# Optimization experiments

Measured on AMD Instinct MI355X. Metric: run time of the kernel, lower is better.

Reference implementation:

```python
import jax, jax.numpy as jnp
import numpy as np

W = 10        # hurst window == signature path window (increments)
DELTA_MAX = 1.5
BN_EPS = 1e-5


def _revcumsum(x, axis):
    return jnp.flip(jnp.cumsum(jnp.flip(x, axis), axis=axis), axis)


def _forward(features, hw1, hb1, hw2, hb2, hw3, hb3, gw1, gb1, gw2, gb2,
             p1, p1b, p2, p2b, p3, p3b, p4, p4b,
             w1, b1, gamma, beta, rmean, rvar, w2, b2, w3, b3):
    B, T, d = features.shape
    f32 = features.dtype
    # log returns, left-padded with 0
    lp = features[:, :, 0]
    ret = jnp.pad(lp[:, 1:] - lp[:, :-1], ((0, 0), (1, 0)))
    # Hurst estimator on sliding windows returns[:, t-W:t] for t in [W, T)
    idxh = jnp.arange(T - W)[:, None] + jnp.arange(W)[None, :]
    rw = ret[:, idxh]                                          # [B, T-W, W]
    hh = jax.nn.relu(rw @ hw1 + hb1)
    hh = jax.nn.relu(hh @ hw2 + hb2)
    H_tail = 0.5 * jax.nn.sigmoid((hh @ hw3 + hb3)[..., 0])    # [B, T-W]
    # first W entries copy the t=W estimate (matches torch slice-broadcast)
    H_local = jnp.concatenate([jnp.repeat(H_tail[:, :1], W, axis=1), H_tail], axis=1)
    vol = jnp.cumsum(jnp.abs(ret), axis=1) / (jnp.arange(1, T + 1, dtype=f32) + 1e-8)
    # depth gate from (H_local, vol_local)
    regime = jnp.stack([H_local, vol], axis=-1)                # [B, T, 2]
    gate = jax.nn.softmax(jax.nn.relu(regime @ gw1 + gb1) @ gw2 + gb2, axis=-1)  # [B,T,4]
    # windowed path increments: window at t covers global increments t-W .. t-1
    Dinc = features[:, 1:] - features[:, :-1]                  # [B, T-1, d]
    Dp = jnp.pad(Dinc, ((0, 0), (W, 0), (0, 0)))
    idx = jnp.arange(T)[:, None] + jnp.arange(W)[None, :]
    Dw = Dp[:, idx]                                            # [B, T, W, d] (zero-padded early)
    S = _revcumsum(Dw, 2)                                      # suffix sums S_r = sum_{m>=r} D_m
    lvl1 = S[:, :, 0]                                          # [B, T, d] = path[-1]-path[0]
    # level2 (torch loop) = sum_{i<=m} D_i (x) D_m  (diagonal included)
    A = Dw[..., :, None] * S[..., None, :]                     # [B, T, W, d, d]
    l2f = jnp.sum(A, axis=2).reshape(B, T, d * d)
    # level3 (torch loop) = sum_{i<j<=n} D_i (x) D_j (x) D_n
    RA = _revcumsum(A, 2) - A                                  # exclusive suffix sum of A
    l3f = jnp.einsum('btrd,btref->btdef', Dw, RA).reshape(B, T, d ** 3)
    # level4 = flatten(level2 (x) level2); (d^2)^2 == d^4 so no pad/trunc
    l4f = (l2f[..., :, None] * l2f[..., None, :]).reshape(B, T, d ** 4)
    proj1 = lvl1 @ p1 + p1b
    proj2 = jnp.concatenate([lvl1, l2f], -1) @ p2 + p2b
    proj3 = jnp.concatenate([lvl1, l2f, l3f], -1) @ p3 + p3b
    proj4 = jnp.concatenate([lvl1, l2f, l3f, l4f], -1) @ p4 + p4b
    # depth k active iff path_len >= k+1 i.e. t >= k (k = depth index)
    tv = jnp.arange(T)
    m2 = (tv >= 1).astype(f32)[None, :, None]
    m3 = (tv >= 2).astype(f32)[None, :, None]
    m4 = (tv >= 3).astype(f32)[None, :, None]
    sig_repr = (gate[..., 0:1] * proj1 + m2 * gate[..., 1:2] * proj2
                + m3 * gate[..., 2:3] * proj3 + m4 * gate[..., 3:4] * proj4)
    combined = jnp.concatenate([sig_repr, features], axis=-1)  # [B, T, h+d]
    h1 = jax.nn.relu(combined @ w1 + b1)
    bn = gamma * (h1 - rmean) * jax.lax.rsqrt(rvar + BN_EPS) + beta  # BatchNorm1d (eval)
    h2 = jax.nn.relu(bn @ w2 + b2)
    return DELTA_MAX * jnp.tanh((h2 @ w3 + b3)[..., 0])        # [B, T]


def setup_inputs() -> dict:
    key = jax.random.key(0)
    ks = jax.random.split(key, 24)
    B, T, d, h = 32, 2048, 5, 64
    def w(k, shape, s=0.1):
        return (jax.random.normal(k, shape) * s).astype(jnp.float32)
    z = lambda n: jnp.zeros((n,), jnp.float32)
    return dict(
        features=0.1 * jax.random.normal(ks[0], (B, T, d), jnp.float32),
        hw1=w(ks[1], (10, 32)), hb1=z(32),
        hw2=w(ks[2], (32, 32)), hb2=z(32),
        hw3=w(ks[3], (32, 1)), hb3=z(1),
        gw1=w(ks[4], (2, 32)), gb1=z(32),
        gw2=w(ks[5], (32, 4)), gb2=z(4),
        p1=w(ks[6], (5, h)), p1b=z(h),
        p2=w(ks[7], (30, h)), p2b=z(h),
        p3=w(ks[8], (155, h)), p3b=z(h),
        p4=w(ks[9], (780, h)), p4b=z(h),
        w1=w(ks[10], (h + d, h)), b1=z(h),
        gamma=jnp.ones((h,), jnp.float32), beta=z(h),
        rmean=0.05 * jax.random.normal(ks[11], (h,), dtype=jnp.float32),
        rvar=jax.random.uniform(ks[12], (h,), jnp.float32, 0.5, 1.5),
        w2=w(ks[13], (h, h // 2)), b2=z(h // 2),
        w3=w(ks[14], (h // 2, 1)), b3=z(1),
    )


def reference(features, hw1, hb1, hw2, hb2, hw3, hb3, gw1, gb1, gw2, gb2,
              p1, p1b, p2, p2b, p3, p3b, p4, p4b,
              w1, b1, gamma, beta, rmean, rvar, w2, b2, w3, b3):
    return _forward(features, hw1, hb1, hw2, hb2, hw3, hb3, gw1, gb1, gw2, gb2,
                    p1, p1b, p2, p2b, p3, p3b, p4, p4b,
                    w1, b1, gamma, beta, rmean, rvar, w2, b2, w3, b3)
```

## Files before the change

### kernel.cpp

```cpp
#include <hip/hip_runtime.h>
#include <math.h>

#define TT 2048
#define W 10

typedef short bf16x8 __attribute__((ext_vector_type(8)));
typedef float f32x4 __attribute__((ext_vector_type(4)));

__device__ __forceinline__ void splitTrunc(float v, unsigned short& hi,
                                           unsigned short& lo) {
  unsigned int u = __float_as_uint(v);
  hi = (unsigned short)(u >> 16);
  float r = v - __uint_as_float(u & 0xffff0000u);
  lo = (unsigned short)(__float_as_uint(r) >> 16);
}

__global__ __launch_bounds__(256) void pre_kernel(
    const float* __restrict__ F,
    const float* __restrict__ hw1, const float* __restrict__ hb1,
    const float* __restrict__ hw2, const float* __restrict__ hb2,
    const float* __restrict__ hw3, const float* __restrict__ hb3,
    const float* __restrict__ gw1, const float* __restrict__ gb1,
    const float* __restrict__ gw2, const float* __restrict__ gb2,
    const float* __restrict__ p1, const float* __restrict__ p2,
    const float* __restrict__ p3, const float* __restrict__ p4,
    unsigned short* __restrict__ WtH, unsigned short* __restrict__ WtL,
    float* __restrict__ gate) {
  const int bid = blockIdx.x;
  const int tid = threadIdx.x;
  if (bid >= 256) {
    int g = (bid - 256) * 256 + tid;
    float v;
    if (g < 2048) {
      int h = g >> 5, k = g & 31;
      v = (k < 5) ? p1[k * 64 + h] : 0.f;
    } else if (g < 4096) {
      int loc = g - 2048, h = loc >> 5, k = loc & 31;
      v = (k < 30) ? p2[k * 64 + h] : 0.f;
    } else if (g < 14336) {
      int loc = g - 4096, h = loc / 160, k = loc - h * 160;
      v = (k < 155) ? p3[k * 64 + h] : 0.f;
    } else {
      int loc = g - 14336, h = loc / 800, k = loc - h * 800;
      if (k < 155) v = p4[k * 64 + h];
      else if (k >= 160 && k < 785) v = p4[(k - 5) * 64 + h];
      else v = 0.f;
    }
    unsigned short hi, lo;
    splitTrunc(v, hi, lo);
    WtH[g] = hi;
    WtL[g] = lo;
    return;
  }
  __shared__ float sRet[TT];
  __shared__ float sCum[TT];
  __shared__ float sPart[256];
  const int b = bid >> 3;
  const int t0 = (bid & 7) << 8;
  const float* fb = F + (size_t)b * TT * 5;
#pragma unroll
  for (int u = 0; u < 8; ++u) {
    int t = u * 256 + tid;
    sRet[t] = (t > 0) ? (fb[t * 5] - fb[(t - 1) * 5]) : 0.f;
  }
  __syncthreads();
  float loc8[8], run = 0.f;
#pragma unroll
  for (int u = 0; u < 8; ++u) {
    run += fabsf(sRet[tid * 8 + u]);
    loc8[u] = run;
  }
  sPart[tid] = run;
  __syncthreads();
  for (int off = 1; off < 256; off <<= 1) {
    float v = (tid >= off) ? sPart[tid - off] : 0.f;
    __syncthreads();
    sPart[tid] += v;
    __syncthreads();
  }
  float excl = sPart[tid] - run;
#pragma unroll
  for (int u = 0; u < 8; ++u) sCum[tid * 8 + u] = excl + loc8[u];
  __syncthreads();
  const int t = t0 + tid;
  const float vv = sCum[t] / ((float)(t + 1) + 1e-8f);
  const int start = (t >= W) ? (t - W) : 0;
  float r[W];
#pragma unroll
  for (int u = 0; u < W; ++u) r[u] = sRet[start + u];
  float h1v[32];
#pragma unroll
  for (int j = 0; j < 32; ++j) {
    float a = hb1[j];
#pragma unroll
    for (int u = 0; u < W; ++u) a = fmaf(r[u], hw1[u * 32 + j], a);
    h1v[j] = fmaxf(a, 0.f);
  }
  float hs = hb3[0];
#pragma unroll
  for (int j = 0; j < 32; ++j) {
    float a = hb2[j];
#pragma unroll
    for (int u = 0; u < 32; ++u) a = fmaf(h1v[u], hw2[u * 32 + j], a);
    hs = fmaf(fmaxf(a, 0.f), hw3[j], hs);
  }
  const float H = 0.5f / (1.f + expf(-hs));
  float l0 = gb2[0], l1 = gb2[1], l2 = gb2[2], l3 = gb2[3];
#pragma unroll
  for (int j = 0; j < 32; ++j) {
    float z = fmaxf(fmaf(H, gw1[j], fmaf(vv, gw1[32 + j], gb1[j])), 0.f);
    l0 = fmaf(z, gw2[j * 4 + 0], l0);
    l1 = fmaf(z, gw2[j * 4 + 1], l1);
    l2 = fmaf(z, gw2[j * 4 + 2], l2);
    l3 = fmaf(z, gw2[j * 4 + 3], l3);
  }
  float m = fmaxf(fmaxf(l0, l1), fmaxf(l2, l3));
  float e0 = expf(l0 - m), e1 = expf(l1 - m), e2 = expf(l2 - m),
        e3 = expf(l3 - m);
  float inv = 1.f / (e0 + e1 + e2 + e3);
  ((float4*)gate)[b * TT + t] = make_float4(e0 * inv, e1 * inv, e2 * inv, e3 * inv);
}

#define MFMA16(a, b, c) __builtin_amdgcn_mfma_f32_16x16x32_bf16((a), (b), (c), 0, 0, 0)

__global__ __launch_bounds__(512, 4) void sig_kernel(
    const float* __restrict__ F, const float* __restrict__ gate,
    const unsigned short* __restrict__ WtH, const unsigned short* __restrict__ WtL,
    const float* __restrict__ p1b, const float* __restrict__ p2b,
    const float* __restrict__ p3b, const float* __restrict__ p4b,
    const float* __restrict__ w1, const float* __restrict__ b1,
    const float* __restrict__ gam, const float* __restrict__ bet,
    const float* __restrict__ rmean, const float* __restrict__ rvar,
    const float* __restrict__ w2, const float* __restrict__ b2,
    const float* __restrict__ w3, const float* __restrict__ b3,
    float* __restrict__ out) {
  __shared__ unsigned short phiH[16][808];
  __shared__ unsigned short phiL[16][808];
  __shared__ __align__(16) float sX[3152];
  __shared__ float sFeat[80];

  float* sDw = sX;
  float* sS = sX + 800;
  float* sL2 = sX + 1600;

  const int tid = threadIdx.x;
  const int posBase = blockIdx.x * 16;

  for (int u = tid; u < 800; u += 512) {
    int p = u / 50, rr = u - p * 50;
    int r = rr / 5, i = rr - r * 5;
    int pos = posBase + p;
    int t = pos & (TT - 1);
    int q = t + r - W;
    float dv = 0.f;
    if (q >= 0) {
      const float* fb = F + (size_t)(pos - t) * 5;
      dv = fb[(q + 1) * 5 + i] - fb[q * 5 + i];
    }
    sDw[u] = dv;
  }
  if (tid < 80) sFeat[tid] = F[(size_t)posBase * 5 + tid];
  __syncthreads();

  if (tid < 80) {
    int p = tid / 5, i = tid - (tid / 5) * 5;
    float s = 0.f;
#pragma unroll
    for (int r = W - 1; r >= 0; --r) {
      s += sDw[p * 50 + r * 5 + i];
      sS[p * 50 + r * 5 + i] = s;
    }
    unsigned short hi, lo;
    splitTrunc(s, hi, lo);
    phiH[p][i] = hi;
    phiL[p][i] = lo;
  }
  __syncthreads();

  if (tid < 400) {
    int p = tid / 25, ef = tid - (tid / 25) * 25;
    int e = ef / 5, fi = ef - e * 5;
    const float* dwp = sDw + p * 50;
    const float* sp = sS + p * 50;
    float a = 0.f;
    float l3a[5] = {0.f, 0.f, 0.f, 0.f, 0.f};
#pragma unroll
    for (int r = W - 1; r >= 0; --r) {
      float aa = a;
#pragma unroll
      for (int i = 0; i < 5; ++i) l3a[i] = fmaf(dwp[r * 5 + i], aa, l3a[i]);
      a = fmaf(dwp[r * 5 + e], sp[r * 5 + fi], a);
    }
    sL2[p * 25 + ef] = a;
    unsigned short hi, lo;
    splitTrunc(a, hi, lo);
    phiH[p][5 + ef] = hi;
    phiL[p][5 + ef] = lo;
#pragma unroll
    for (int i = 0; i < 5; ++i) {
      splitTrunc(l3a[i], hi, lo);
      phiH[p][30 + i * 25 + ef] = hi;
      phiL[p][30 + i * 25 + ef] = lo;
    }
  }
  if (tid < 320) {
    int p = tid / 20, mm = tid - (tid / 20) * 20;
    int kk = (mm < 5) ? (155 + mm) : (780 + mm);
    phiH[p][kk] = 0;
    phiL[p][kk] = 0;
  }
  __syncthreads();

  {
    int p = tid >> 5, t32 = tid & 31;
    int base = t32 * 20;
    int count = (t32 == 31) ? 5 : 20;
    const float* l2p = sL2 + p * 25;
    int i = base / 25, j = base - i * 25;
    unsigned short* rowH = &phiH[p][160 + base];
    unsigned short* rowL = &phiL[p][160 + base];
    int mEnd = count & ~1;
    for (int m = 0; m < mEnd; m += 2) {
      float v0 = l2p[i] * l2p[j];
      j++; if (j == 25) { j = 0; i++; }
      float v1 = l2p[i] * l2p[j];
      j++; if (j == 25) { j = 0; i++; }
      unsigned short h0, lo0, h1, lo1;
      splitTrunc(v0, h0, lo0);
      splitTrunc(v1, h1, lo1);
      *(unsigned int*)(rowH + m) = (unsigned int)h0 | ((unsigned int)h1 << 16);
      *(unsigned int*)(rowL + m) = (unsigned int)lo0 | ((unsigned int)lo1 << 16);
    }
    if (count & 1) {
      float v0 = l2p[i] * l2p[j];
      unsigned short h0, lo0;
      splitTrunc(v0, h0, lo0);
      rowH[mEnd] = h0;
      rowL[mEnd] = lo0;
    }
  }
  __syncthreads();

  const int lane = tid & 63;
  const int wvAll = tid >> 6;
  const int ht = wvAll & 3, kg = wvAll >> 2;
  const int col = lane & 15, quad = lane >> 4;
  const int hw = ht * 16;
  const int arow = hw + col;

  const unsigned short* bHp = &phiH[col][quad * 8];
  const unsigned short* bLp = &phiL[col][quad * 8];
  const unsigned short* a4H = WtH + 14336 + arow * 800 + quad * 8;
  const unsigned short* a4L = WtL + 14336 + arow * 800 + quad * 8;

  f32x4 acc4a = {0.f, 0.f, 0.f, 0.f}, acc4b = {0.f, 0.f, 0.f, 0.f};
  f32x4 acc3a = {0.f, 0.f, 0.f, 0.f}, acc3b = {0.f, 0.f, 0.f, 0.f};
  f32x4 acc2 = {0.f, 0.f, 0.f, 0.f}, acc1 = {0.f, 0.f, 0.f, 0.f};

  if (kg == 0) {
    for (int s = 0; s < 16; ++s) {
      bf16x8 bh = *(const bf16x8*)(bHp + s * 32);
      bf16x8 bl = *(const bf16x8*)(bLp + s * 32);
      bf16x8 ah = *(const bf16x8*)(a4H + s * 32);
      bf16x8 al = *(const bf16x8*)(a4L + s * 32);
      acc4a = MFMA16(ah, bh, acc4a);
      acc4b = MFMA16(ah, bl, acc4b);
      acc4b = MFMA16(al, bh, acc4b);
    }
  } else {
    for (int s = 16; s < 25; ++s) {
      bf16x8 bh = *(const bf16x8*)(bHp + s * 32);
      bf16x8 bl = *(const bf16x8*)(bLp + s * 32);
      bf16x8 ah = *(const bf16x8*)(a4H + s * 32);
      bf16x8 al = *(const bf16x8*)(a4L + s * 32);
      acc4a = MFMA16(ah, bh, acc4a);
      acc4b = MFMA16(ah, bl, acc4b);
      acc4b = MFMA16(al, bh, acc4b);
    }
    const unsigned short* a3H = WtH + 4096 + arow * 160 + quad * 8;
    const unsigned short* a3L = WtL + 4096 + arow * 160 + quad * 8;
    for (int s = 0; s < 5; ++s) {
      bf16x8 bh = *(const bf16x8*)(bHp + s * 32);
      bf16x8 bl = *(const bf16x8*)(bLp + s * 32);
      bf16x8 ch = *(const bf16x8*)(a3H + s * 32);
      bf16x8 cl = *(const bf16x8*)(a3L + s * 32);
      acc3a = MFMA16(ch, bh, acc3a);
      acc3b = MFMA16(ch, bl, acc3b);
      acc3b = MFMA16(cl, bh, acc3b);
    }
    bf16x8 bh0 = *(const bf16x8*)(bHp);
    bf16x8 bl0 = *(const bf16x8*)(bLp);
    const unsigned short* a2H = WtH + 2048 + arow * 32 + quad * 8;
    const unsigned short* a2L = WtL + 2048 + arow * 32 + quad * 8;
    bf16x8 dh = *(const bf16x8*)a2H;
    bf16x8 dl = *(const bf16x8*)a2L;
    acc2 = MFMA16(dh, bh0, acc2);
    acc2 = MFMA16(dh, bl0, acc2);
    acc2 = MFMA16(dl, bh0, acc2);
    const unsigned short* a1H = WtH + arow * 32 + quad * 8;
    const unsigned short* a1L = WtL + arow * 32 + quad * 8;
    bf16x8 eh = *(const bf16x8*)a1H;
    bf16x8 el = *(const bf16x8*)a1L;
    acc1 = MFMA16(eh, bh0, acc1);
    acc1 = MFMA16(eh, bl0, acc1);
    acc1 = MFMA16(el, bh0, acc1);
  }

  const int pos = posBase + col;
  const int t = pos & (TT - 1);
  float4 g = ((const float4*)gate)[pos];
  const float g0 = g.x;
  const float g1 = (t >= 1) ? g.y : 0.f;
  const float g2 = (t >= 2) ? g.z : 0.f;
  const float g3 = (t >= 3) ? g.w : 0.f;

  if (kg == 1) {
    f32x4 a4 = acc4a + acc4b;
    f32x4 a3 = acc3a + acc3b;
    f32x4 v;
#pragma unroll
    for (int r = 0; r < 4; ++r)
      v[r] = g0 * acc1[r] + g1 * acc2[r] + g2 * a3[r] + g3 * a4[r];
    *(f32x4*)&sX[(ht * 64 + lane) * 4] = v;
  }
  __syncthreads();
  if (kg == 0) {
    f32x4 a4 = acc4a + acc4b;
    f32x4 vo = *(const f32x4*)&sX[(ht * 64 + lane) * 4];
    float* sSig = sX + 1024;
#pragma unroll
    for (int r = 0; r < 4; ++r) {
      int h = hw + quad * 4 + r;
      float bias = g0 * p1b[h] + g1 * p2b[h] + g2 * p3b[h] + g3 * p4b[h];
      sSig[col * 68 + h] = vo[r] + g3 * a4[r] + bias;
    }
  }
  __syncthreads();

  {
    const float* sSig = sX + 1024;
    float* sBn = sX + 2112;
    const int j = lane;
    const int pA = wvAll * 2, pB = pA + 1;
    float a0 = b1[j], a1 = a0;
    const float* sg0 = sSig + pA * 68;
    const float* sg1 = sSig + pB * 68;
    for (int i = 0; i < 64; ++i) {
      float wt = w1[i * 64 + j];
      a0 = fmaf(sg0[i], wt, a0);
      a1 = fmaf(sg1[i], wt, a1);
    }
#pragma unroll
    for (int i = 0; i < 5; ++i) {
      float wt = w1[(64 + i) * 64 + j];
      a0 = fmaf(sFeat[pA * 5 + i], wt, a0);
      a1 = fmaf(sFeat[pB * 5 + i], wt, a1);
    }
    float sc = gam[j] * rsqrtf(rvar[j] + 1e-5f);
    float rm = rmean[j], be = bet[j];
    sBn[pA * 65 + j] = fmaf(fmaxf(a0, 0.f) - rm, sc, be);
    sBn[pB * 65 + j] = fmaf(fmaxf(a1, 0.f) - rm, sc, be);
  }
  __syncthreads();

  {
    const float* sBn = sX + 2112;
    const float b3s = b3[0];
    int p = tid >> 5, k = tid & 31;
    const float* bnp = sBn + p * 65;
    float a = b2[k];
    for (int jj = 0; jj < 64; ++jj) a = fmaf(bnp[jj], w2[jj * 32 + k], a);
    float partial = fmaxf(a, 0.f) * w3[k];
#pragma unroll
    for (int off = 16; off >= 1; off >>= 1) partial += __shfl_xor(partial, off, 32);
    if (k == 0) out[posBase + p] = 1.5f * tanhf(partial + b3s);
  }
}

extern "C" void kernel_launch(void* const* d_in, const int* in_sizes, int n_in,
                              void* d_out, int out_size, void* d_ws, size_t ws_size,
                              hipStream_t stream) {
  const float* F = (const float*)d_in[0];
  const float* hw1 = (const float*)d_in[1];
  const float* hb1 = (const float*)d_in[2];
  const float* hw2 = (const float*)d_in[3];
  const float* hb2 = (const float*)d_in[4];
  const float* hw3 = (const float*)d_in[5];
  const float* hb3 = (const float*)d_in[6];
  const float* gw1 = (const float*)d_in[7];
  const float* gb1 = (const float*)d_in[8];
  const float* gw2 = (const float*)d_in[9];
  const float* gb2 = (const float*)d_in[10];
  const float* p1 = (const float*)d_in[11];
  const float* p1b = (const float*)d_in[12];
  const float* p2 = (const float*)d_in[13];
  const float* p2b = (const float*)d_in[14];
  const float* p3 = (const float*)d_in[15];
  const float* p3b = (const float*)d_in[16];
  const float* p4 = (const float*)d_in[17];
  const float* p4b = (const float*)d_in[18];
  const float* w1 = (const float*)d_in[19];
  const float* b1 = (const float*)d_in[20];
  const float* gam = (const float*)d_in[21];
  const float* bet = (const float*)d_in[22];
  const float* rmean = (const float*)d_in[23];
  const float* rvar = (const float*)d_in[24];
  const float* w2 = (const float*)d_in[25];
  const float* b2 = (const float*)d_in[26];
  const float* w3 = (const float*)d_in[27];
  const float* b3 = (const float*)d_in[28];

  float* ws = (float*)d_ws;
  float* gate = ws;
  unsigned short* WtH = (unsigned short*)(ws + 262144);
  unsigned short* WtL = WtH + 65536;
  float* out = (float*)d_out;

  pre_kernel<<<512, 256, 0, stream>>>(F, hw1, hb1, hw2, hb2, hw3, hb3, gw1,
                                      gb1, gw2, gb2, p1, p2, p3, p4, WtH, WtL,
                                      gate);
  sig_kernel<<<4096, 512, 0, stream>>>(F, gate, WtH, WtL, p1b, p2b, p3b, p4b,
                                       w1, b1, gam, bet, rmean, rvar, w2, b2,
                                       w3, b3, out);
}
```

Measured before the change: 241.7 us.

## Exploit symmetry of level-2 outer product to halve level-4 GEMM K dimension

The level-4 signature features are the outer product of the level-2 vector with itself, which is symmetric. The p4 weights are therefore folded so only 13 of the 25 cyclic diagonals are used, shrinking the K dimension from 800 to 512 and cutting LDS and MFMA work. Signature levels are now computed from raw features in registers with one wave per position, and the l2xl2 products are built with cross-lane shuffles. The change also removes a sync stage, shrinks LDS to allow 6 blocks per CU, and switches the bf16 hi/lo split from truncation to round-to-nearest.

Result: slower. 253.3 us (+4.8%).

```diff
diff --git a/kernel.cpp b/kernel.cpp
--- a/kernel.cpp
+++ b/kernel.cpp
@@ -7,13 +7,24 @@
 typedef short bf16x8 __attribute__((ext_vector_type(8)));
 typedef float f32x4 __attribute__((ext_vector_type(4)));
 
-__device__ __forceinline__ void splitTrunc(float v, unsigned short& hi,
-                                           unsigned short& lo) {
+#define MFMA16(a, b, c) __builtin_amdgcn_mfma_f32_16x16x32_bf16((a), (b), (c), 0, 0, 0)
+
+__device__ __forceinline__ unsigned short rneBf16(float v) {
   unsigned int u = __float_as_uint(v);
-  hi = (unsigned short)(u >> 16);
-  float r = v - __uint_as_float(u & 0xffff0000u);
-  lo = (unsigned short)(__float_as_uint(r) >> 16);
-}
+  u += 0x7FFFu + ((u >> 16) & 1u);
+  return (unsigned short)(u >> 16);
+}
+__device__ __forceinline__ void splitRne(float v, unsigned short& hi,
+                                         unsigned short& lo) {
+  hi = rneBf16(v);
+  float r = v - __uint_as_float((unsigned int)hi << 16);
+  lo = rneBf16(r);
+}
+
+#define OFF_W2 2048
+#define OFF_W3 4096
+#define OFF_W4 14336
+#define WT_TOTAL 47104
 
 __global__ __launch_bounds__(256) void pre_kernel(
     const float* __restrict__ F,
@@ -41,13 +52,22 @@
       int loc = g - 4096, h = loc / 160, k = loc - h * 160;
       v = (k < 155) ? p3[k * 64 + h] : 0.f;
     } else {
-      int loc = g - 14336, h = loc / 800, k = loc - h * 800;
-      if (k < 155) v = p4[k * 64 + h];
-      else if (k >= 160 && k < 785) v = p4[(k - 5) * 64 + h];
-      else v = 0.f;
+      int loc = g - 14336, h = loc >> 9, k = loc & 511;
+      if (k < 155) {
+        v = p4[k * 64 + h];
+      } else if (k >= 160 && k < 485) {
+        int kap = k - 160;
+        int c = kap / 25, mm = kap - c * 25;
+        int jj = mm + c;
+        if (jj >= 25) jj -= 25;
+        v = p4[(155 + mm * 25 + jj) * 64 + h];
+        if (c > 0) v += p4[(155 + jj * 25 + mm) * 64 + h];
+      } else {
+        v = 0.f;
+      }
     }
     unsigned short hi, lo;
-    splitTrunc(v, hi, lo);
+    splitRne(v, hi, lo);
     WtH[g] = hi;
     WtL[g] = lo;
     return;
@@ -121,9 +141,44 @@
   ((float4*)gate)[b * TT + t] = make_float4(e0 * inv, e1 * inv, e2 * inv, e3 * inv);
 }
 
-#define MFMA16(a, b, c) __builtin_amdgcn_mfma_f32_16x16x32_bf16((a), (b), (c), 0, 0, 0)
-
-__global__ __launch_bounds__(512, 4) void sig_kernel(
+template <bool GUARD>
+static __device__ __forceinline__ void sigCore(const float* sR, int p, int e,
+                                               int fi, float* l3a, float& aout,
+                                               float& sout) {
+  int b10 = (p + 10) * 5;
+  float h0 = sR[b10 + 0], h1 = sR[b10 + 1], h2 = sR[b10 + 2], h3 = sR[b10 + 3],
+        h4 = sR[b10 + 4];
+  float hiE = sR[b10 + e], hiF = sR[b10 + fi];
+  float a = 0.f, sfi = 0.f;
+  float l0 = 0.f, l1 = 0.f, l2 = 0.f, l3 = 0.f, l4 = 0.f;
+#pragma unroll
+  for (int r = 9; r >= 0; --r) {
+    const int base = (p + r) * 5;
+    float n0 = sR[base + 0], n1 = sR[base + 1], n2 = sR[base + 2],
+          n3 = sR[base + 3], n4 = sR[base + 4];
+    float nE = sR[base + e], nF = sR[base + fi];
+    float d0 = h0 - n0, d1 = h1 - n1, d2 = h2 - n2, d3 = h3 - n3, d4 = h4 - n4;
+    float dE = hiE - nE, dF = hiF - nF;
+    if (GUARD) {
+      float vm = ((p + r) >= 10) ? 1.f : 0.f;
+      d0 *= vm; d1 *= vm; d2 *= vm; d3 *= vm; d4 *= vm; dE *= vm; dF *= vm;
+    }
+    sfi += dF;
+    float aa = a;
+    l0 = fmaf(d0, aa, l0);
+    l1 = fmaf(d1, aa, l1);
+    l2 = fmaf(d2, aa, l2);
+    l3 = fmaf(d3, aa, l3);
+    l4 = fmaf(d4, aa, l4);
+    a = fmaf(dE, sfi, a);
+    h0 = n0; h1 = n1; h2 = n2; h3 = n3; h4 = n4; hiE = nE; hiF = nF;
+  }
+  l3a[0] = l0; l3a[1] = l1; l3a[2] = l2; l3a[3] = l3; l3a[4] = l4;
+  aout = a;
+  sout = sfi;
+}
+
+__global__ __launch_bounds__(512, 6) void sig_kernel(
     const float* __restrict__ F, const float* __restrict__ gate,
     const unsigned short* __restrict__ WtH, const unsigned short* __restrict__ WtL,
     const float* __restrict__ p1b, const float* __restrict__ p2b,
@@ -134,164 +189,141 @@
     const float* __restrict__ w2, const float* __restrict__ b2,
     const float* __restrict__ w3, const float* __restrict__ b3,
     float* __restrict__ out) {
-  __shared__ unsigned short phiH[16][808];
-  __shared__ unsigned short phiL[16][808];
-  __shared__ __align__(16) float sX[3152];
-  __shared__ float sFeat[80];
-
-  float* sDw = sX;
-  float* sS = sX + 800;
-  float* sL2 = sX + 1600;
+  __shared__ __align__(16) unsigned short phiH[16][520];
+  __shared__ __align__(16) unsigned short phiL[16][520];
+  __shared__ float sRaw[132];
 
   const int tid = threadIdx.x;
   const int posBase = blockIdx.x * 16;
-
-  for (int u = tid; u < 800; u += 512) {
-    int p = u / 50, rr = u - p * 50;
-    int r = rr / 5, i = rr - r * 5;
-    int pos = posBase + p;
-    int t = pos & (TT - 1);
-    int q = t + r - W;
-    float dv = 0.f;
-    if (q >= 0) {
-      const float* fb = F + (size_t)(pos - t) * 5;
-      dv = fb[(q + 1) * 5 + i] - fb[q * 5 + i];
-    }
-    sDw[u] = dv;
-  }
-  if (tid < 80) sFeat[tid] = F[(size_t)posBase * 5 + tid];
-  __syncthreads();
-
-  if (tid < 80) {
-    int p = tid / 5, i = tid - (tid / 5) * 5;
-    float s = 0.f;
-#pragma unroll
-    for (int r = W - 1; r >= 0; --r) {
-      s += sDw[p * 50 + r * 5 + i];
-      sS[p * 50 + r * 5 + i] = s;
-    }
-    unsigned short hi, lo;
-    splitTrunc(s, hi, lo);
-    phiH[p][i] = hi;
-    phiL[p][i] = lo;
-  }
-  __syncthreads();
-
-  if (tid < 400) {
-    int p = tid / 25, ef = tid - (tid / 25) * 25;
-    int e = ef / 5, fi = ef - e * 5;
-    const float* dwp = sDw + p * 50;
-    const float* sp = sS + p * 50;
-    float a = 0.f;
-    float l3a[5] = {0.f, 0.f, 0.f, 0.f, 0.f};
-#pragma unroll
-    for (int r = W - 1; r >= 0; --r) {
-      float aa = a;
-#pragma unroll
-      for (int i = 0; i < 5; ++i) l3a[i] = fmaf(dwp[r * 5 + i], aa, l3a[i]);
-      a = fmaf(dwp[r * 5 + e], sp[r * 5 + fi], a);
-    }
-    sL2[p * 25 + ef] = a;
-    unsigned short hi, lo;
-    splitTrunc(a, hi, lo);
-    phiH[p][5 + ef] = hi;
-    phiL[p][5 + ef] = lo;
-#pragma unroll
-    for (int i = 0; i < 5; ++i) {
-      splitTrunc(l3a[i], hi, lo);
-      phiH[p][30 + i * 25 + ef] = hi;
-      phiL[p][30 + i * 25 + ef] = lo;
-    }
-  }
-  if (tid < 320) {
-    int p = tid / 20, mm = tid - (tid / 20) * 20;
-    int kk = (mm < 5) ? (155 + mm) : (780 + mm);
+  const int t0 = posBase & (TT - 1);
+
+  {
+    int p = tid >> 5, mm = tid & 31;
+    int kk = (mm < 5) ? (155 + mm) : (480 + mm);
     phiH[p][kk] = 0;
     phiL[p][kk] = 0;
   }
-  __syncthreads();
-
-  {
-    int p = tid >> 5, t32 = tid & 31;
-    int base = t32 * 20;
-    int count = (t32 == 31) ? 5 : 20;
-    const float* l2p = sL2 + p * 25;
-    int i = base / 25, j = base - i * 25;
-    unsigned short* rowH = &phiH[p][160 + base];
-    unsigned short* rowL = &phiL[p][160 + base];
-    int mEnd = count & ~1;
-    for (int m = 0; m < mEnd; m += 2) {
-      float v0 = l2p[i] * l2p[j];
-      j++; if (j == 25) { j = 0; i++; }
-      float v1 = l2p[i] * l2p[j];
-      j++; if (j == 25) { j = 0; i++; }
-      unsigned short h0, lo0, h1, lo1;
-      splitTrunc(v0, h0, lo0);
-      splitTrunc(v1, h1, lo1);
-      *(unsigned int*)(rowH + m) = (unsigned int)h0 | ((unsigned int)h1 << 16);
-      *(unsigned int*)(rowL + m) = (unsigned int)lo0 | ((unsigned int)lo1 << 16);
-    }
-    if (count & 1) {
-      float v0 = l2p[i] * l2p[j];
-      unsigned short h0, lo0;
-      splitTrunc(v0, h0, lo0);
-      rowH[mEnd] = h0;
-      rowL[mEnd] = lo0;
+  if (tid < 130) {
+    const float* fb = F + (size_t)(posBase - t0) * 5;
+    int idx = (t0 - W) * 5 + tid;
+    sRaw[tid] = (idx >= 0) ? fb[idx] : 0.f;
+  }
+  __syncthreads();
+
+  const int pgrp = tid >> 5;
+  const int m = tid & 31;
+  float l2v = 0.f;
+  if (m < 25) {
+    const int e = m / 5;
+    const int fi = m - e * 5;
+    float l3a[5], a, sfi;
+    if (t0 != 0)
+      sigCore<false>(sRaw, pgrp, e, fi, l3a, a, sfi);
+    else
+      sigCore<true>(sRaw, pgrp, e, fi, l3a, a, sfi);
+    l2v = a;
+    unsigned short hi, lo;
+    if (m < 5) {
+      splitRne(sfi, hi, lo);
+      phiH[pgrp][m] = hi;
+      phiL[pgrp][m] = lo;
+    }
+    splitRne(a, hi, lo);
+    phiH[pgrp][5 + m] = hi;
+    phiL[pgrp][5 + m] = lo;
+#pragma unroll
+    for (int i = 0; i < 5; ++i) {
+      splitRne(l3a[i], hi, lo);
+      phiH[pgrp][30 + i * 25 + m] = hi;
+      phiL[pgrp][30 + i * 25 + m] = lo;
+    }
+  }
+  const int laneBase = tid & 32;
+#pragma unroll
+  for (int c = 0; c < 13; ++c) {
+    int j = m + c;
+    if (j >= 25) j -= 25;
+    float other = __shfl(l2v, laneBase + j, 64);
+    if (m < 25) {
+      unsigned short hi, lo;
+      splitRne(l2v * other, hi, lo);
+      phiH[pgrp][160 + c * 25 + m] = hi;
+      phiL[pgrp][160 + c * 25 + m] = lo;
     }
   }
   __syncthreads();
 
   const int lane = tid & 63;
-  const int wvAll = tid >> 6;
-  const int ht = wvAll & 3, kg = wvAll >> 2;
+  const int wv = tid >> 6;
+  const int ht = wv & 3, kg = wv >> 2;
   const int col = lane & 15, quad = lane >> 4;
   const int hw = ht * 16;
   const int arow = hw + col;
 
   const unsigned short* bHp = &phiH[col][quad * 8];
   const unsigned short* bLp = &phiL[col][quad * 8];
-  const unsigned short* a4H = WtH + 14336 + arow * 800 + quad * 8;
-  const unsigned short* a4L = WtL + 14336 + arow * 800 + quad * 8;
-
-  f32x4 acc4a = {0.f, 0.f, 0.f, 0.f}, acc4b = {0.f, 0.f, 0.f, 0.f};
-  f32x4 acc3a = {0.f, 0.f, 0.f, 0.f}, acc3b = {0.f, 0.f, 0.f, 0.f};
-  f32x4 acc2 = {0.f, 0.f, 0.f, 0.f}, acc1 = {0.f, 0.f, 0.f, 0.f};
-
+  const unsigned short* a4H = WtH + OFF_W4 + arow * 512 + quad * 8;
+  const unsigned short* a4L = WtL + OFF_W4 + arow * 512 + quad * 8;
+
+  const int pos = posBase + col;
+  const int t = pos & (TT - 1);
+  float4 g = ((const float4*)gate)[pos];
+  const float g0 = g.x;
+  const float g1 = (t >= 1) ? g.y : 0.f;
+  const float g2 = (t >= 2) ? g.z : 0.f;
+  const float g3 = (t >= 3) ? g.w : 0.f;
+
+  f32x4 res;
   if (kg == 0) {
-    for (int s = 0; s < 16; ++s) {
+    f32x4 t4a = {0.f, 0.f, 0.f, 0.f}, t4b = {0.f, 0.f, 0.f, 0.f};
+    for (int s = 0; s < 12; ++s) {
       bf16x8 bh = *(const bf16x8*)(bHp + s * 32);
       bf16x8 bl = *(const bf16x8*)(bLp + s * 32);
       bf16x8 ah = *(const bf16x8*)(a4H + s * 32);
       bf16x8 al = *(const bf16x8*)(a4L + s * 32);
-      acc4a = MFMA16(ah, bh, acc4a);
-      acc4b = MFMA16(ah, bl, acc4b);
-      acc4b = MFMA16(al, bh, acc4b);
-    }
+      t4a = MFMA16(ah, bh, t4a);
+      t4b = MFMA16(ah, bl, t4b);
+      t4b = MFMA16(al, bh, t4b);
+    }
+    f32x4 a4 = t4a + t4b;
+    const int hq = hw + quad * 4;
+    f32x4 b1v = *(const f32x4*)(p1b + hq);
+    f32x4 b2v = *(const f32x4*)(p2b + hq);
+    f32x4 b3v = *(const f32x4*)(p3b + hq);
+    f32x4 b4v = *(const f32x4*)(p4b + hq);
+#pragma unroll
+    for (int r = 0; r < 4; ++r)
+      res[r] = g3 * a4[r] + g0 * b1v[r] + g1 * b2v[r] + g2 * b3v[r] + g3 * b4v[r];
   } else {
-    for (int s = 16; s < 25; ++s) {
+    f32x4 t4a = {0.f, 0.f, 0.f, 0.f}, t4b = {0.f, 0.f, 0.f, 0.f};
+    for (int s = 12; s < 16; ++s) {
       bf16x8 bh = *(const bf16x8*)(bHp + s * 32);
       bf16x8 bl = *(const bf16x8*)(bLp + s * 32);
       bf16x8 ah = *(const bf16x8*)(a4H + s * 32);
       bf16x8 al = *(const bf16x8*)(a4L + s * 32);
-      acc4a = MFMA16(ah, bh, acc4a);
-      acc4b = MFMA16(ah, bl, acc4b);
-      acc4b = MFMA16(al, bh, acc4b);
-    }
-    const unsigned short* a3H = WtH + 4096 + arow * 160 + quad * 8;
-    const unsigned short* a3L = WtL + 4096 + arow * 160 + quad * 8;
+      t4a = MFMA16(ah, bh, t4a);
+      t4b = MFMA16(ah, bl, t4b);
+      t4b = MFMA16(al, bh, t4b);
+    }
+    f32x4 a4 = t4a + t4b;
+    const unsigned short* a3H = WtH + OFF_W3 + arow * 160 + quad * 8;
+    const unsigned short* a3L = WtL + OFF_W3 + arow * 160 + quad * 8;
+    f32x4 t3a = {0.f, 0.f, 0.f, 0.f}, t3b = {0.f, 0.f, 0.f, 0.f};
     for (int s = 0; s < 5; ++s) {
       bf16x8 bh = *(const bf16x8*)(bHp + s * 32);
       bf16x8 bl = *(const bf16x8*)(bLp + s * 32);
       bf16x8 ch = *(const bf16x8*)(a3H + s * 32);
       bf16x8 cl = *(const bf16x8*)(a3L + s * 32);
-      acc3a = MFMA16(ch, bh, acc3a);
-      acc3b = MFMA16(ch, bl, acc3b);
-      acc3b = MFMA16(cl, bh, acc3b);
-    }
+      t3a = MFMA16(ch, bh, t3a);
+      t3b = MFMA16(ch, bl, t3b);
+      t3b = MFMA16(cl, bh, t3b);
+    }
+    f32x4 a3 = t3a + t3b;
     bf16x8 bh0 = *(const bf16x8*)(bHp);
     bf16x8 bl0 = *(const bf16x8*)(bLp);
-    const unsigned short* a2H = WtH + 2048 + arow * 32 + quad * 8;
-    const unsigned short* a2L = WtL + 2048 + arow * 32 + quad * 8;
+    f32x4 acc2 = {0.f, 0.f, 0.f, 0.f}, acc1 = {0.f, 0.f, 0.f, 0.f};
+    const unsigned short* a2H = WtH + OFF_W2 + arow * 32 + quad * 8;
+    const unsigned short* a2L = WtL + OFF_W2 + arow * 32 + quad * 8;
     bf16x8 dh = *(const bf16x8*)a2H;
     bf16x8 dl = *(const bf16x8*)a2L;
     acc2 = MFMA16(dh, bh0, acc2);
@@ -304,70 +336,55 @@
     acc1 = MFMA16(eh, bh0, acc1);
     acc1 = MFMA16(eh, bl0, acc1);
     acc1 = MFMA16(el, bh0, acc1);
-  }
-
-  const int pos = posBase + col;
-  const int t = pos & (TT - 1);
-  float4 g = ((const float4*)gate)[pos];
-  const float g0 = g.x;
-  const float g1 = (t >= 1) ? g.y : 0.f;
-  const float g2 = (t >= 2) ? g.z : 0.f;
-  const float g3 = (t >= 3) ? g.w : 0.f;
-
-  if (kg == 1) {
-    f32x4 a4 = acc4a + acc4b;
-    f32x4 a3 = acc3a + acc3b;
-    f32x4 v;
 #pragma unroll
     for (int r = 0; r < 4; ++r)
-      v[r] = g0 * acc1[r] + g1 * acc2[r] + g2 * a3[r] + g3 * a4[r];
-    *(f32x4*)&sX[(ht * 64 + lane) * 4] = v;
-  }
-  __syncthreads();
-  if (kg == 0) {
-    f32x4 a4 = acc4a + acc4b;
-    f32x4 vo = *(const f32x4*)&sX[(ht * 64 + lane) * 4];
-    float* sSig = sX + 1024;
-#pragma unroll
-    for (int r = 0; r < 4; ++r) {
-      int h = hw + quad * 4 + r;
-      float bias = g0 * p1b[h] + g1 * p2b[h] + g2 * p3b[h] + g3 * p4b[h];
-      sSig[col * 68 + h] = vo[r] + g3 * a4[r] + bias;
-    }
-  }
-  __syncthreads();
-
+      res[r] = g0 * acc1[r] + g1 * acc2[r] + g2 * a3[r] + g3 * a4[r];
+  }
+
+  __syncthreads();
+
+  float* sSigA = (float*)&phiH[0][0];
+  float* sSigB = sSigA + 16 * 66;
   {
-    const float* sSig = sX + 1024;
-    float* sBn = sX + 2112;
+    float* dst = (kg == 0) ? sSigA : sSigB;
+    const int hq = hw + quad * 4;
+#pragma unroll
+    for (int r = 0; r < 4; ++r) dst[col * 66 + hq + r] = res[r];
+  }
+  __syncthreads();
+
+  {
     const int j = lane;
-    const int pA = wvAll * 2, pB = pA + 1;
+    const int pA = wv * 2, pB = pA + 1;
     float a0 = b1[j], a1 = a0;
-    const float* sg0 = sSig + pA * 68;
-    const float* sg1 = sSig + pB * 68;
+    const float* sA0 = sSigA + pA * 66;
+    const float* sB0 = sSigB + pA * 66;
+    const float* sA1 = sSigA + pB * 66;
+    const float* sB1 = sSigB + pB * 66;
     for (int i = 0; i < 64; ++i) {
       float wt = w1[i * 64 + j];
-      a0 = fmaf(sg0[i], wt, a0);
-      a1 = fmaf(sg1[i], wt, a1);
+      a0 = fmaf(sA0[i] + sB0[i], wt, a0);
+      a1 = fmaf(sA1[i] + sB1[i], wt, a1);
     }
 #pragma unroll
     for (int i = 0; i < 5; ++i) {
       float wt = w1[(64 + i) * 64 + j];
-      a0 = fmaf(sFeat[pA * 5 + i], wt, a0);
-      a1 = fmaf(sFeat[pB * 5 + i], wt, a1);
+      a0 = fmaf(sRaw[(10 + pA) * 5 + i], wt, a0);
+      a1 = fmaf(sRaw[(10 + pB) * 5 + i], wt, a1);
     }
     float sc = gam[j] * rsqrtf(rvar[j] + 1e-5f);
     float rm = rmean[j], be = bet[j];
-    sBn[pA * 65 + j] = fmaf(fmaxf(a0, 0.f) - rm, sc, be);
-    sBn[pB * 65 + j] = fmaf(fmaxf(a1, 0.f) - rm, sc, be);
+    float* sBn = (float*)&phiL[0][0];
+    sBn[pA * 64 + j] = fmaf(fmaxf(a0, 0.f) - rm, sc, be);
+    sBn[pB * 64 + j] = fmaf(fmaxf(a1, 0.f) - rm, sc, be);
   }
   __syncthreads();
 
   {
-    const float* sBn = sX + 2112;
+    const float* sBn = (const float*)&phiL[0][0];
     const float b3s = b3[0];
     int p = tid >> 5, k = tid & 31;
-    const float* bnp = sBn + p * 65;
+    const float* bnp = sBn + p * 64;
     float a = b2[k];
     for (int jj = 0; jj < 64; ++jj) a = fmaf(bnp[jj], w2[jj * 32 + k], a);
     float partial = fmaxf(a, 0.f) * w3[k];
@@ -413,10 +430,10 @@
   float* ws = (float*)d_ws;
   float* gate = ws;
   unsigned short* WtH = (unsigned short*)(ws + 262144);
-  unsigned short* WtL = WtH + 65536;
+  unsigned short* WtL = WtH + WT_TOTAL;
   float* out = (float*)d_out;
 
-  pre_kernel<<<512, 256, 0, stream>>>(F, hw1, hb1, hw2, hb2, hw3, hb3, gw1,
+  pre_kernel<<<440, 256, 0, stream>>>(F, hw1, hb1, hw2, hb2, hw3, hb3, gw1,
                                       gb1, gw2, gb2, p1, p2, p3, p4, WtH, WtL,
                                       gate);
   sig_kernel<<<4096, 512, 0, stream>>>(F, gate, WtH, WtL, p1b, p2b, p3b, p4b,
```
